# Kernel optimization log

Hardware: AMD Instinct MI355X
Metric: run time of the kernel (lower is better)

The kernel has to match this reference:

```python
import jax, jax.numpy as jnp
import numpy as np

HIDDEN = 512
VOCAB = 32000
BATCH = 64
SEQ = 256
N_LAYERS = 2
MAXLEN = 32


def setup_inputs() -> dict:
    key = jax.random.key(0)
    ks = jax.random.split(key, 8)
    s = 1.0 / np.sqrt(HIDDEN)
    return {
        "x": jax.random.randint(ks[0], (BATCH, SEQ), 0, VOCAB, dtype=jnp.int64),
        "emb": jax.random.normal(ks[1], (VOCAB, HIDDEN), jnp.float32),
        "W_ih": jax.random.uniform(ks[2], (N_LAYERS, HIDDEN, HIDDEN), jnp.float32, -s, s),
        "W_hh": jax.random.uniform(ks[3], (N_LAYERS, HIDDEN, HIDDEN), jnp.float32, -s, s),
        "b_ih": jax.random.uniform(ks[4], (N_LAYERS, HIDDEN), jnp.float32, -s, s),
        "b_hh": jax.random.uniform(ks[5], (N_LAYERS, HIDDEN), jnp.float32, -s, s),
        "W_fc": jax.random.uniform(ks[6], (VOCAB, HIDDEN), jnp.float32, -s, s),
        "b_fc": jax.random.uniform(ks[7], (VOCAB,), jnp.float32, -s, s),
    }


def _cell(h, x_t, W_ih, W_hh, b_ih, b_hh):
    # h: [L, B, H] stacked hidden; x_t: [B, H]. Multi-layer tanh Elman step.
    n_layers = W_ih.shape[0]
    inp = x_t
    new_h = []
    for l in range(n_layers):  # small fixed layer count
        hl = jnp.tanh(inp @ W_ih[l].T + b_ih[l] + h[l] @ W_hh[l].T + b_hh[l])
        new_h.append(hl)
        inp = hl
    return jnp.stack(new_h), inp


def reference(x, emb, W_ih, W_hh, b_ih, b_hh, W_fc, b_fc):
    B = x.shape[0]
    # ---- encoder: embed tokens, run stacked RNN over time ----
    xe = emb[x]  # [B, S, H]
    h0 = jnp.zeros((W_ih.shape[0], B, HIDDEN), emb.dtype)

    def enc_step(h, xt):
        h2, out = _cell(h, xt, W_ih, W_hh, b_ih, b_hh)
        return h2, out

    h_enc, _ = jax.lax.scan(enc_step, h0, jnp.swapaxes(xe, 0, 1))

    tok0 = jnp.zeros((B,), jnp.int32)

    def dec_step(carry, _):
        h, tok = carry
        e = emb[tok]  # [B, H]
        h2, out = _cell(h, e, W_ih, W_hh, b_ih, b_hh)
        logits = out @ W_fc.T + b_fc  # [B, V]
        nxt = jnp.argmax(logits, axis=-1).astype(jnp.int32)
        return (h2, nxt), logits

    (h_fin, _), logits = jax.lax.scan(dec_step, (h_enc, tok0), None, length=MAXLEN)
    vec_out = jnp.swapaxes(logits, 0, 1)  # [B, MAXLEN, V]
    return vec_out, h_fin
```

## Files before the change

### kernel.cpp

```cpp
#include <hip/hip_runtime.h>
#include <hip/hip_bf16.h>


typedef float v4f __attribute__((ext_vector_type(4)));
typedef short short8 __attribute__((ext_vector_type(8)));
typedef unsigned long long u64;

#define HID 512
#define NBAT 64
#define SEQL 256
#define NV 32000
#define TDEC 32
#define BH (64 * 512)
#define FPAD 32

__device__ __forceinline__ unsigned short f2bf(float f) {
  unsigned u = __float_as_uint(f);
  u = u + 0x7FFFu + ((u >> 16) & 1u);
  return (unsigned short)(u >> 16);
}
__device__ __forceinline__ unsigned fenc(float f) {
  unsigned u = __float_as_uint(f);
  return (u & 0x80000000u) ? ~u : (u | 0x80000000u);
}
__device__ __forceinline__ float ldf(const float* p) {
  return __hip_atomic_load(p, __ATOMIC_RELAXED, __HIP_MEMORY_SCOPE_AGENT);
}
__device__ __forceinline__ void stf(float* p, float v) {
  __hip_atomic_store(p, v, __ATOMIC_RELAXED, __HIP_MEMORY_SCOPE_AGENT);
}
__device__ __forceinline__ int ldflag(const int* p) {
  return __hip_atomic_load(p, __ATOMIC_RELAXED, __HIP_MEMORY_SCOPE_AGENT);
}
__device__ __forceinline__ void stflag(int* p, int v) {
  __hip_atomic_store(p, v, __ATOMIC_RELAXED, __HIP_MEMORY_SCOPE_AGENT);
}

__device__ __forceinline__ void wgbar(int* flags, int wg, int first, int count, unsigned ep) {
  __atomic_signal_fence(__ATOMIC_SEQ_CST);
  __builtin_amdgcn_s_waitcnt(0);
  __syncthreads();
  const int tid = threadIdx.x;
  if (tid == 0) stflag(&flags[wg * FPAD], (int)ep);
  int* rel = &flags[(256 + (first >> 5) + (count == 256 ? 8 : 0)) * FPAD];
  if (wg == first) {
    if (tid < 64) {
      for (int f = first + tid; f < first + count; f += 64) {
        while ((unsigned)ldflag(&flags[f * FPAD]) < ep) __builtin_amdgcn_s_sleep(1);
      }
    }
    __syncthreads();
    if (tid == 0) stflag(rel, (int)ep);
  } else if (tid == 0) {
    while ((unsigned)ldflag(rel) < ep) __builtin_amdgcn_s_sleep(4);
  }
  __atomic_signal_fence(__ATOMIC_SEQ_CST);
  __syncthreads();
}

__global__ void k_wfcb(const float* __restrict__ W, unsigned short* __restrict__ Wb) {
  const int n = NV * HID;
  for (int i = ((int)blockIdx.x * 256 + (int)threadIdx.x) * 8; i < n; i += 2048 * 256 * 8) {
    v4f a = *(const v4f*)(W + i);
    v4f b = *(const v4f*)(W + i + 4);
    short8 o;
    o[0] = (short)f2bf(a[0]); o[1] = (short)f2bf(a[1]);
    o[2] = (short)f2bf(a[2]); o[3] = (short)f2bf(a[3]);
    o[4] = (short)f2bf(b[0]); o[5] = (short)f2bf(b[1]);
    o[6] = (short)f2bf(b[2]); o[7] = (short)f2bf(b[3]);
    *(short8*)(Wb + i) = o;
  }
}

template <int GATHER>
__global__ __launch_bounds__(256, 2) void k_gemm(const float* __restrict__ A,
                                                 const int* __restrict__ xtok,
                                                 const float* __restrict__ emb,
                                                 const float* __restrict__ W,
                                                 const float* __restrict__ bias,
                                                 float* __restrict__ P) {
  __shared__ __align__(16) float As[32 * 132];
  __shared__ __align__(16) float Bs[32 * 132];
  const int tid = threadIdx.x;
  const int i0 = ((int)blockIdx.x >> 2) * 128, j0 = ((int)blockIdx.x & 3) * 128;
  const int tx = tid & 15, ty = tid >> 4;
  float acc[8][8] = {};
  const int sa = 4 * ((tx >> 2) & 1);
  const int sb = 4 * ((ty >> 2) & 1);
  const int pa0 = (tx * 8) ^ sa, pa1 = (tx * 8 + 4) ^ sa;
  const int pb0 = (ty * 8) ^ sb, pb1 = (ty * 8 + 4) ^ sb;
  for (int kc = 0; kc < HID; kc += 32) {
#pragma unroll
    for (int u = 0; u < 4; u++) {
      int lin = tid + u * 256;
      int il = lin >> 3, kq = (lin & 7) * 4;
      int pi = il ^ (4 * ((il >> 5) & 1));
      const float* asrc;
      if (GATHER) {
        int row = i0 + il;
        int tok = xtok[(row & 63) * SEQL + (row >> 6)];
        asrc = emb + (size_t)tok * HID + kc + kq;
      } else {
        asrc = A + (size_t)(i0 + il) * HID + kc + kq;
      }
      v4f av = *(const v4f*)asrc;
      v4f bv = *(const v4f*)(W + (size_t)(j0 + il) * HID + kc + kq);
      As[(kq + 0) * 132 + pi] = av[0]; As[(kq + 1) * 132 + pi] = av[1];
      As[(kq + 2) * 132 + pi] = av[2]; As[(kq + 3) * 132 + pi] = av[3];
      Bs[(kq + 0) * 132 + pi] = bv[0]; Bs[(kq + 1) * 132 + pi] = bv[1];
      Bs[(kq + 2) * 132 + pi] = bv[2]; Bs[(kq + 3) * 132 + pi] = bv[3];
    }
    __syncthreads();
#pragma unroll 8
    for (int k = 0; k < 32; k++) {
      v4f a0 = *(const v4f*)&As[k * 132 + pa0];
      v4f a1 = *(const v4f*)&As[k * 132 + pa1];
      v4f b0 = *(const v4f*)&Bs[k * 132 + pb0];
      v4f b1 = *(const v4f*)&Bs[k * 132 + pb1];
      float ar[8] = {a0[0], a0[1], a0[2], a0[3], a1[0], a1[1], a1[2], a1[3]};
      float br[8] = {b0[0], b0[1], b0[2], b0[3], b1[0], b1[1], b1[2], b1[3]};
#pragma unroll
      for (int r = 0; r < 8; r++)
#pragma unroll
        for (int c = 0; c < 8; c++) acc[r][c] = fmaf(ar[r], br[c], acc[r][c]);
    }
    __syncthreads();
  }
  v4f bl0 = *(const v4f*)(bias + j0 + ty * 8);
  v4f bl1 = *(const v4f*)(bias + j0 + ty * 8 + 4);
#pragma unroll
  for (int r = 0; r < 8; r++) {
    float* dst = P + (size_t)(i0 + tx * 8 + r) * HID + j0 + ty * 8;
    v4f o0 = {acc[r][0] + bl0[0], acc[r][1] + bl0[1], acc[r][2] + bl0[2], acc[r][3] + bl0[3]};
    v4f o1 = {acc[r][4] + bl1[0], acc[r][5] + bl1[1], acc[r][6] + bl1[2], acc[r][7] + bl1[3]};
    *(v4f*)dst = o0;
    *(v4f*)(dst + 4) = o1;
  }
}

__global__ __launch_bounds__(256, 2) void k_scan(float* __restrict__ P,
                                                 const float* __restrict__ Whh,
                                                 const float* __restrict__ bhh,
                                                 float* __restrict__ hbuf,
                                                 int* __restrict__ flags, int store_h,
                                                 unsigned ep) {
  __shared__ __align__(16) float hs[32 * 132];
  const int wg = blockIdx.x, tid = threadIdx.x;
  const int bg = wg >> 5, jg = wg & 31;
  const int b0 = bg * 8, j0 = jg * 16;
  const int bh = tid & 1, jg2 = (tid >> 1) & 3, ks = tid >> 3;
  v4f wv[4][4];
#pragma unroll
  for (int jj = 0; jj < 4; jj++)
#pragma unroll
    for (int i4 = 0; i4 < 4; i4++)
      wv[jj][i4] = *(const v4f*)(Whh + (size_t)(j0 + jg2 * 4 + jj) * HID + ks * 16 + i4 * 4);
  for (int t = 0; t < SEQL; t++) {
    const int p = t & 1;
    float* Pt = P + (size_t)t * BH;
    const float* hsrc = hbuf + p * BH + b0 * HID;
#pragma unroll
    for (int u = 0; u < 16; u++) {
      int lin = tid + u * 256;
      int b = lin >> 9, k = lin & 511;
      hs[(k >> 4) * 132 + b * 16 + (k & 15)] = ldf(hsrc + b * HID + k);
    }
    __syncthreads();
    float acc[4][4] = {};
#pragma unroll
    for (int i4 = 0; i4 < 4; i4++) {
#pragma unroll
      for (int bb = 0; bb < 4; bb++) {
        int b = bh * 4 + bb;
        v4f hv = *(const v4f*)&hs[ks * 132 + b * 16 + i4 * 4];
#pragma unroll
        for (int jj = 0; jj < 4; jj++) {
          float a = acc[bb][jj];
          a = fmaf(hv[0], wv[jj][i4][0], a);
          a = fmaf(hv[1], wv[jj][i4][1], a);
          a = fmaf(hv[2], wv[jj][i4][2], a);
          a = fmaf(hv[3], wv[jj][i4][3], a);
          acc[bb][jj] = a;
        }
      }
    }
    __syncthreads();
#pragma unroll
    for (int bb = 0; bb < 4; bb++) {
      v4f pv = {acc[bb][0], acc[bb][1], acc[bb][2], acc[bb][3]};
      *(v4f*)&hs[ks * 132 + (bh * 4 + bb) * 16 + jg2 * 4] = pv;
    }
    __syncthreads();
    if (tid < 128) {
      int bb = tid >> 4, jj = tid & 15;
      float sum = 0.f;
#pragma unroll
      for (int k2 = 0; k2 < 32; k2++) sum += hs[k2 * 132 + bb * 16 + jj];
      int jglob = j0 + jj, bglob = b0 + bb;
      float z = Pt[bglob * HID + jglob] + bhh[jglob] + sum;
      float h = tanhf(z);
      stf(&hbuf[(p ^ 1) * BH + bglob * HID + jglob], h);
      if (store_h) Pt[bglob * HID + jglob] = h;
    }
    wgbar(flags, wg, bg * 32, 32, ++ep);
  }
}

__device__ __forceinline__ void issue_tile(const unsigned short* __restrict__ Wfcb,
                                           float* buf, int wg, int tid, int T) {
  const int wv = tid >> 6, ln = tid & 63;
  const unsigned short* sb =
      Wfcb + (size_t)(wg * 128 + wv * 32 + (ln & 15)) * HID + T * 128 + (ln >> 4) * 8;
#pragma unroll
  for (int kc = 0; kc < 4; kc++)
#pragma unroll
    for (int fq = 0; fq < 2; fq++)
      __builtin_amdgcn_global_load_lds(
          (const unsigned int*)(sb + (size_t)fq * 16 * HID + kc * 32),
          (unsigned int*)(buf + wv * 2048 + kc * 512 + fq * 256), 16, 0, 0);
}

template <int PH>
__global__ __launch_bounds__(256, 1) void k_cell(
    const float* __restrict__ emb, const float* __restrict__ Wih,
    const float* __restrict__ Whh, const float* __restrict__ bih,
    const float* __restrict__ bhh, const u64* __restrict__ best,
    float* __restrict__ h0buf, float* __restrict__ h1buf,
    unsigned short* __restrict__ h1bf, int st) {
  __shared__ __align__(16) float Wl[2 * 4224];
  __shared__ __align__(16) float es[32 * 268];
  __shared__ __align__(16) float hss[32 * 268];
  const int wg = blockIdx.x, tid = threadIdx.x;
  const int bg = wg >> 6, jgD = wg & 63;
  const int bh = tid & 3, jg2 = (tid >> 2) & 1, ks = tid >> 3;
  const int p = st & 1;
#pragma unroll
  for (int m = 0; m < 2; m++) {
    const float* src = (m ? Whh : Wih) + (size_t)PH * HID * HID;
#pragma unroll
    for (int u = 0; u < 4; u++) {
      int lin = tid + u * 256;
      int j = lin >> 7, k4 = (lin & 127) * 4;
      v4f v = *(const v4f*)(src + (size_t)(jgD * 8 + j) * HID + k4);
      *(v4f*)&Wl[m * 4224 + (k4 >> 4) * 132 + j * 16 + (k4 & 15)] = v;
    }
  }
  if (PH == 0) {
#pragma unroll
    for (int u = 0; u < 8; u++) {
      int lin = tid + u * 256;
      int b = lin >> 7, k4 = (lin & 127) * 4;
      unsigned vtok = 0u;
      if (st > 0) {
        u64 kk = best[bg * 16 + b];
        vtok = 0xFFFFFFFFu - (unsigned)(kk & 0xFFFFFFFFull);
        if (vtok >= (unsigned)NV) vtok = 0u;
      }
      v4f av = *(const v4f*)(emb + (size_t)vtok * HID + k4);
      *(v4f*)&es[(k4 >> 4) * 268 + b * 16 + (k4 & 15)] = av;
    }
#pragma unroll
    for (int u = 0; u < 32; u++) {
      int lin = tid + u * 256;
      int b = lin >> 9, k = lin & 511;
      hss[(k >> 4) * 268 + b * 16 + (k & 15)] = h0buf[p * BH + (bg * 16 + b) * HID + k];
    }
  } else {
#pragma unroll
    for (int u = 0; u < 32; u++) {
      int lin = tid + u * 256;
      int b = lin >> 9, k = lin & 511;
      int off = (k >> 4) * 268 + b * 16 + (k & 15);
      int row = (bg * 16 + b) * HID + k;
      es[off] = h0buf[(p ^ 1) * BH + row];
      hss[off] = h1buf[p * BH + row];
    }
  }
  __syncthreads();
  float acc[4][4] = {};
  const float* Wi = &Wl[0];
  const float* Wh = &Wl[4224];
#pragma unroll
  for (int i4 = 0; i4 < 4; i4++) {
    v4f wi[4], wh[4];
#pragma unroll
    for (int jj = 0; jj < 4; jj++) {
      wi[jj] = *(const v4f*)&Wi[ks * 132 + (jg2 * 4 + jj) * 16 + i4 * 4];
      wh[jj] = *(const v4f*)&Wh[ks * 132 + (jg2 * 4 + jj) * 16 + i4 * 4];
    }
#pragma unroll
    for (int bb = 0; bb < 4; bb++) {
      int b = bh * 4 + bb;
      v4f evv = *(const v4f*)&es[ks * 268 + b * 16 + i4 * 4];
      v4f hvv = *(const v4f*)&hss[ks * 268 + b * 16 + i4 * 4];
#pragma unroll
      for (int jj = 0; jj < 4; jj++) {
        float a = acc[bb][jj];
        a = fmaf(evv[0], wi[jj][0], a); a = fmaf(evv[1], wi[jj][1], a);
        a = fmaf(evv[2], wi[jj][2], a); a = fmaf(evv[3], wi[jj][3], a);
        a = fmaf(hvv[0], wh[jj][0], a); a = fmaf(hvv[1], wh[jj][1], a);
        a = fmaf(hvv[2], wh[jj][2], a); a = fmaf(hvv[3], wh[jj][3], a);
        acc[bb][jj] = a;
      }
    }
  }
  __syncthreads();
#pragma unroll
  for (int bb = 0; bb < 4; bb++) {
    v4f pv = {acc[bb][0], acc[bb][1], acc[bb][2], acc[bb][3]};
    *(v4f*)&es[ks * 132 + (bh * 4 + bb) * 8 + jg2 * 4] = pv;
  }
  __syncthreads();
  if (tid < 128) {
    int b = tid >> 3, j = tid & 7;
    float sum = 0.f;
#pragma unroll
    for (int k2 = 0; k2 < 32; k2++) sum += es[k2 * 132 + b * 8 + j];
    int jglob = jgD * 8 + j, bglob = bg * 16 + b;
    float z = bih[PH * HID + jglob] + bhh[PH * HID + jglob] + sum;
    float h = tanhf(z);
    float* hb = (PH ? h1buf : h0buf);
    hb[(p ^ 1) * BH + bglob * HID + jglob] = h;
    if (PH) {
      unsigned hbv = f2bf(h);
      unsigned nb = (unsigned)__shfl_down((int)hbv, 1);
      if ((j & 1) == 0)
        *(unsigned*)(h1bf + (size_t)bglob * HID + jglob) = hbv | (nb << 16);
    }
  }
}

__global__ __launch_bounds__(256, 1) void k_logits(
    const unsigned short* __restrict__ Wfcb, const unsigned short* __restrict__ h1bf,
    const float* __restrict__ bfc, float* __restrict__ out, float* __restrict__ pmaxp,
    u64* __restrict__ best, int st) {
  __shared__ __align__(16) float tb0[8192];
  __shared__ __align__(16) float tb1[8192];
  __shared__ float pmr[256];
  const int wg = blockIdx.x, tid = threadIdx.x;
  if (wg == 250) {
    if (tid < 64) best[tid] = 0ull;
    return;
  }
  const int w = tid >> 6, lane = tid & 63;
  const int l16 = lane & 15, quad = lane >> 4;
  const int n0 = wg * 128 + w * 32;
  const int nc0 = n0 + l16, nc1 = n0 + 16 + l16;
  const float bf0 = bfc[nc0], bf1 = bfc[nc1];
  issue_tile(Wfcb, tb0, wg, tid, 0);
  v4f acc[4][2] = {};
#pragma unroll
  for (int t = 0; t < 4; t++) {
    __builtin_amdgcn_sched_barrier(0);
    const float* buf = (t & 1) ? tb1 : tb0;
    union { u64 q[2]; short8 s; } au[4][4];
#pragma unroll
    for (int mb = 0; mb < 4; mb++) {
      const unsigned short* hr = h1bf + (size_t)(mb * 16 + l16) * HID + t * 128 + quad * 8;
#pragma unroll
      for (int kc = 0; kc < 4; kc++) {
        au[mb][kc].q[0] = *(const u64*)(hr + kc * 32);
        au[mb][kc].q[1] = *(const u64*)(hr + kc * 32 + 4);
      }
    }
    __builtin_amdgcn_sched_barrier(0);
    if (t < 3) issue_tile(Wfcb, (t & 1) ? tb0 : tb1, wg, tid, t + 1);
    __builtin_amdgcn_sched_barrier(0);
    if (t < 3) asm volatile("s_waitcnt vmcnt(8)" ::: "memory");
    else       asm volatile("s_waitcnt vmcnt(0)" ::: "memory");
    __builtin_amdgcn_sched_barrier(0);
#pragma unroll
    for (int kc = 0; kc < 4; kc++) {
      short8 b0 = *(const short8*)(buf + w * 2048 + kc * 512 + lane * 4);
      short8 b1 = *(const short8*)(buf + w * 2048 + kc * 512 + 256 + lane * 4);
#pragma unroll
      for (int mb = 0; mb < 4; mb++) {
        acc[mb][0] =
            __builtin_amdgcn_mfma_f32_16x16x32_bf16(au[mb][kc].s, b0, acc[mb][0], 0, 0, 0);
        acc[mb][1] =
            __builtin_amdgcn_mfma_f32_16x16x32_bf16(au[mb][kc].s, b1, acc[mb][1], 0, 0, 0);
      }
    }
  }
#pragma unroll
  for (int mb = 0; mb < 4; mb++) {
#pragma unroll
    for (int r = 0; r < 4; r++) {
      float v0 = acc[mb][0][r] + bf0;
      float v1 = acc[mb][1][r] + bf1;
      int m = mb * 16 + quad * 4 + r;
      out[(size_t)(m * TDEC + st) * NV + nc0] = v0;
      out[(size_t)(m * TDEC + st) * NV + nc1] = v1;
      float mx = fmaxf(v0, v1);
      mx = fmaxf(mx, __shfl_xor(mx, 1));
      mx = fmaxf(mx, __shfl_xor(mx, 2));
      mx = fmaxf(mx, __shfl_xor(mx, 4));
      mx = fmaxf(mx, __shfl_xor(mx, 8));
      if (l16 == 0) pmr[w * 64 + m] = mx;
    }
  }
  __syncthreads();
  if (tid < 64) {
    float m4 = fmaxf(fmaxf(pmr[tid], pmr[64 + tid]), fmaxf(pmr[128 + tid], pmr[192 + tid]));
    pmaxp[tid * 256 + wg] = m4;
  }
}

__global__ __launch_bounds__(256, 1) void k_argmax(
    const float* __restrict__ Wfc, const float* __restrict__ bfc,
    const float* __restrict__ h1buf, const float* __restrict__ pmaxp,
    const float* __restrict__ out, u64* __restrict__ best, int st) {
  __shared__ __align__(16) float hcache[512];
  __shared__ float red[256];
  const int wg = blockIdx.x, tid = threadIdx.x;
  const int b = wg >> 2, q = wg & 3;
  const int p = st & 1;
  const float* hrow = h1buf + (p ^ 1) * BH + b * HID;
  hcache[tid] = hrow[tid];
  hcache[tid + 256] = hrow[tid + 256];
  red[tid] = (tid < 250) ? pmaxp[b * 256 + tid] : -3.0e38f;
  __syncthreads();
  for (int o = 128; o > 0; o >>= 1) {
    if (tid < o) red[tid] = fmaxf(red[tid], red[tid + o]);
    __syncthreads();
  }
  const float thr = red[0] - 0.05f;
  const size_t ob = (size_t)(b * TDEC + st) * NV + q * 8000;
  for (int i = tid * 2; i < 8000; i += 512) {
    u64 qq = *(const u64*)(out + ob + i);
    float lv[2] = {__uint_as_float((unsigned)qq), __uint_as_float((unsigned)(qq >> 32))};
#pragma unroll
    for (int c = 0; c < 2; c++) {
      if (lv[c] >= thr) {
        int vidx = q * 8000 + i + c;
        const v4f* h4 = (const v4f*)hcache;
        const v4f* w4 = (const v4f*)(Wfc + (size_t)vidx * HID);
        v4f s0 = 0, s1 = 0;
        for (int k = 0; k < 128; k += 2) {
          s0 += h4[k] * w4[k];
          s1 += h4[k + 1] * w4[k + 1];
        }
        v4f sv = s0 + s1;
        float d = bfc[vidx] + sv[0] + sv[1] + sv[2] + sv[3];
        u64 key = ((u64)fenc(d) << 32) | (u64)(0xFFFFFFFFu - (unsigned)vidx);
        atomicMax(&best[b], key);
      }
    }
  }
}

__global__ void k_hfin(const float* __restrict__ h0buf, const float* __restrict__ h1buf,
                       float* __restrict__ out) {
  int lin = (int)blockIdx.x * 256 + (int)threadIdx.x;
  int l = lin >> 15, r2 = lin & 32767;
  out[65536000 + lin] = (l ? h1buf : h0buf)[r2];
}

extern "C" void kernel_launch(void* const* d_in, const int* in_sizes, int n_in, void* d_out,
                              int out_size, void* d_ws, size_t ws_size, hipStream_t stream) {
  const int* x = (const int*)d_in[0];
  const float* emb = (const float*)d_in[1];
  const float* Wih = (const float*)d_in[2];
  const float* Whh = (const float*)d_in[3];
  const float* bih = (const float*)d_in[4];
  const float* bhh = (const float*)d_in[5];
  const float* Wfc = (const float*)d_in[6];
  const float* bfc = (const float*)d_in[7];
  float* out = (float*)d_out;
  char* ws = (char*)d_ws;

  float* P0 = (float*)ws;
  float* P1 = P0 + (size_t)SEQL * BH;
  unsigned short* Wfcb = (unsigned short*)(P1 + (size_t)SEQL * BH);
  char* small = (char*)(Wfcb + (size_t)NV * HID);
  float* h0buf = (float*)small;
  float* h1buf = h0buf + 2 * BH;
  unsigned short* h1bf = (unsigned short*)(h1buf + 2 * BH);
  float* pmaxp = (float*)(h1bf + BH);
  u64* best = (u64*)(pmaxp + 256 * 64);
  int* flags = (int*)(best + 64);
  size_t small_bytes = (size_t)2 * BH * 4 + (size_t)2 * BH * 4 + BH * 2 + 256 * 64 * 4 +
                       64 * 8 + (256 + 16) * FPAD * 4;

  hipMemsetAsync(small, 0, small_bytes, stream);
  k_wfcb<<<2048, 256, 0, stream>>>(Wfc, Wfcb);
  k_gemm<1><<<512, 256, 0, stream>>>(nullptr, x, emb, Wih, bih, P0);
  k_scan<<<256, 256, 0, stream>>>(P0, Whh, bhh, h0buf, flags, 1, 0u);
  k_gemm<0><<<512, 256, 0, stream>>>(P0, nullptr, nullptr, Wih + 262144, bih + 512, P1);
  k_scan<<<256, 256, 0, stream>>>(P1, Whh + 262144, bhh + 512, h1buf, flags, 0, 256u);
  for (int st = 0; st < TDEC; st++) {
    k_cell<0><<<256, 256, 0, stream>>>(emb, Wih, Whh, bih, bhh, best, h0buf, h1buf, h1bf, st);
    k_cell<1><<<256, 256, 0, stream>>>(emb, Wih, Whh, bih, bhh, best, h0buf, h1buf, h1bf, st);
    k_logits<<<251, 256, 0, stream>>>(Wfcb, h1bf, bfc, out, pmaxp, best, st);
    k_argmax<<<256, 256, 0, stream>>>(Wfc, bfc, h1buf, pmaxp, out, best, st);
  }
  k_hfin<<<256, 256, 0, stream>>>(h0buf, h1buf, out);
}
```

Before: 6.529 ms.

## Fuse both encoder RNN layers into one wavefront-pipelined persistent scan kernel

Replaces the two sequential layer scans and the intermediate layer-1 input GEMM with a single 512-workgroup persistent kernel. Layer 0 workgroups write hidden states into a 4-slot ring, and layer 1 workgroups consume them one step behind, computing the W_ih projection inline. Cross-layer flags give backpressure so the ring is not overwritten. This overlaps the two serial recurrences and removes a GEMM launch plus the P1 traffic. In exchange, layer 1 does extra per-step work, and the kernel relies on all 512 workgroups being co-resident for the spin barriers.

```diff
diff --git a/kernel.cpp b/kernel.cpp
--- a/kernel.cpp
+++ b/kernel.cpp
@@ -34,28 +34,6 @@
 }
 __device__ __forceinline__ void stflag(int* p, int v) {
   __hip_atomic_store(p, v, __ATOMIC_RELAXED, __HIP_MEMORY_SCOPE_AGENT);
-}
-
-__device__ __forceinline__ void wgbar(int* flags, int wg, int first, int count, unsigned ep) {
-  __atomic_signal_fence(__ATOMIC_SEQ_CST);
-  __builtin_amdgcn_s_waitcnt(0);
-  __syncthreads();
-  const int tid = threadIdx.x;
-  if (tid == 0) stflag(&flags[wg * FPAD], (int)ep);
-  int* rel = &flags[(256 + (first >> 5) + (count == 256 ? 8 : 0)) * FPAD];
-  if (wg == first) {
-    if (tid < 64) {
-      for (int f = first + tid; f < first + count; f += 64) {
-        while ((unsigned)ldflag(&flags[f * FPAD]) < ep) __builtin_amdgcn_s_sleep(1);
-      }
-    }
-    __syncthreads();
-    if (tid == 0) stflag(rel, (int)ep);
-  } else if (tid == 0) {
-    while ((unsigned)ldflag(rel) < ep) __builtin_amdgcn_s_sleep(4);
-  }
-  __atomic_signal_fence(__ATOMIC_SEQ_CST);
-  __syncthreads();
 }
 
 __global__ void k_wfcb(const float* __restrict__ W, unsigned short* __restrict__ Wb) {
@@ -138,71 +116,198 @@
   }
 }
 
-__global__ __launch_bounds__(256, 2) void k_scan(float* __restrict__ P,
-                                                 const float* __restrict__ Whh,
-                                                 const float* __restrict__ bhh,
-                                                 float* __restrict__ hbuf,
-                                                 int* __restrict__ flags, int store_h,
-                                                 unsigned ep) {
-  __shared__ __align__(16) float hs[32 * 132];
-  const int wg = blockIdx.x, tid = threadIdx.x;
+__global__ __launch_bounds__(256, 2) void k_scan2(
+    const float* __restrict__ P0, const float* __restrict__ Wih,
+    const float* __restrict__ Whh, const float* __restrict__ bih,
+    const float* __restrict__ bhh, float* __restrict__ h0ring,
+    float* __restrict__ h0buf, float* __restrict__ h1buf, int* __restrict__ flags) {
+  __shared__ __align__(16) float hs0[32 * 132];
+  __shared__ __align__(16) float hs1[32 * 132];
+  const int wgid = blockIdx.x, tid = threadIdx.x;
+  const int layer = wgid >> 8;
+  const int wg = wgid & 255;
   const int bg = wg >> 5, jg = wg & 31;
   const int b0 = bg * 8, j0 = jg * 16;
   const int bh = tid & 1, jg2 = (tid >> 1) & 3, ks = tid >> 3;
-  v4f wv[4][4];
-#pragma unroll
-  for (int jj = 0; jj < 4; jj++)
-#pragma unroll
-    for (int i4 = 0; i4 < 4; i4++)
-      wv[jj][i4] = *(const v4f*)(Whh + (size_t)(j0 + jg2 * 4 + jj) * HID + ks * 16 + i4 * 4);
-  for (int t = 0; t < SEQL; t++) {
-    const int p = t & 1;
-    float* Pt = P + (size_t)t * BH;
-    const float* hsrc = hbuf + p * BH + b0 * HID;
-#pragma unroll
-    for (int u = 0; u < 16; u++) {
-      int lin = tid + u * 256;
-      int b = lin >> 9, k = lin & 511;
-      hs[(k >> 4) * 132 + b * 16 + (k & 15)] = ldf(hsrc + b * HID + k);
-    }
-    __syncthreads();
-    float acc[4][4] = {};
-#pragma unroll
-    for (int i4 = 0; i4 < 4; i4++) {
+  int* arr = &flags[wgid * FPAD];
+  int* relA = &flags[(512 + bg) * FPAD];
+  int* relB = &flags[(520 + bg) * FPAD];
+
+  if (layer == 0) {
+    v4f wv[4][4];
+#pragma unroll
+    for (int jj = 0; jj < 4; jj++)
+#pragma unroll
+      for (int i4 = 0; i4 < 4; i4++)
+        wv[jj][i4] = *(const v4f*)(Whh + (size_t)(j0 + jg2 * 4 + jj) * HID + ks * 16 + i4 * 4);
+    for (int t = 0; t < SEQL; t++) {
+      const float* hsrc = h0ring + ((t + 3) & 3) * BH + b0 * HID;
+#pragma unroll
+      for (int u = 0; u < 16; u++) {
+        int lin = tid + u * 256;
+        int b = lin >> 9, k = lin & 511;
+        hs0[(k >> 4) * 132 + b * 16 + (k & 15)] = ldf(hsrc + b * HID + k);
+      }
+      __syncthreads();
+      float acc[4][4] = {};
+#pragma unroll
+      for (int i4 = 0; i4 < 4; i4++) {
+#pragma unroll
+        for (int bb = 0; bb < 4; bb++) {
+          int b = bh * 4 + bb;
+          v4f hv = *(const v4f*)&hs0[ks * 132 + b * 16 + i4 * 4];
+#pragma unroll
+          for (int jj = 0; jj < 4; jj++) {
+            float a = acc[bb][jj];
+            a = fmaf(hv[0], wv[jj][i4][0], a);
+            a = fmaf(hv[1], wv[jj][i4][1], a);
+            a = fmaf(hv[2], wv[jj][i4][2], a);
+            a = fmaf(hv[3], wv[jj][i4][3], a);
+            acc[bb][jj] = a;
+          }
+        }
+      }
+      __syncthreads();
 #pragma unroll
       for (int bb = 0; bb < 4; bb++) {
-        int b = bh * 4 + bb;
-        v4f hv = *(const v4f*)&hs[ks * 132 + b * 16 + i4 * 4];
-#pragma unroll
-        for (int jj = 0; jj < 4; jj++) {
-          float a = acc[bb][jj];
-          a = fmaf(hv[0], wv[jj][i4][0], a);
-          a = fmaf(hv[1], wv[jj][i4][1], a);
-          a = fmaf(hv[2], wv[jj][i4][2], a);
-          a = fmaf(hv[3], wv[jj][i4][3], a);
-          acc[bb][jj] = a;
+        v4f pv = {acc[bb][0], acc[bb][1], acc[bb][2], acc[bb][3]};
+        *(v4f*)&hs0[ks * 132 + (bh * 4 + bb) * 16 + jg2 * 4] = pv;
+      }
+      __syncthreads();
+      if (tid < 128) {
+        int bb = tid >> 4, jj = tid & 15;
+        float sum = 0.f;
+#pragma unroll
+        for (int k2 = 0; k2 < 32; k2++) sum += hs0[k2 * 132 + bb * 16 + jj];
+        int jglob = j0 + jj, bglob = b0 + bb;
+        float z = P0[(size_t)t * BH + bglob * HID + jglob] + bhh[jglob] + sum;
+        float h = tanhf(z);
+        stf(&h0ring[(t & 3) * BH + bglob * HID + jglob], h);
+        if (t == SEQL - 1) stf(&h0buf[bglob * HID + jglob], h);
+      }
+      unsigned ep = (unsigned)(t + 1);
+      __atomic_signal_fence(__ATOMIC_SEQ_CST);
+      __builtin_amdgcn_s_waitcnt(0);
+      __syncthreads();
+      if (tid == 0) stflag(arr, (int)ep);
+      if (jg == 0) {
+        if (tid < 32) {
+          while ((unsigned)ldflag(&flags[(bg * 32 + tid) * FPAD]) < ep)
+            __builtin_amdgcn_s_sleep(1);
+        } else if (tid == 32 && ep > 3) {
+          while ((unsigned)ldflag(relB) < ep - 3) __builtin_amdgcn_s_sleep(1);
         }
-      }
-    }
-    __syncthreads();
-#pragma unroll
-    for (int bb = 0; bb < 4; bb++) {
-      v4f pv = {acc[bb][0], acc[bb][1], acc[bb][2], acc[bb][3]};
-      *(v4f*)&hs[ks * 132 + (bh * 4 + bb) * 16 + jg2 * 4] = pv;
-    }
-    __syncthreads();
-    if (tid < 128) {
-      int bb = tid >> 4, jj = tid & 15;
-      float sum = 0.f;
-#pragma unroll
-      for (int k2 = 0; k2 < 32; k2++) sum += hs[k2 * 132 + bb * 16 + jj];
-      int jglob = j0 + jj, bglob = b0 + bb;
-      float z = Pt[bglob * HID + jglob] + bhh[jglob] + sum;
-      float h = tanhf(z);
-      stf(&hbuf[(p ^ 1) * BH + bglob * HID + jglob], h);
-      if (store_h) Pt[bglob * HID + jglob] = h;
-    }
-    wgbar(flags, wg, bg * 32, 32, ++ep);
+        __syncthreads();
+        if (tid == 0) stflag(relA, (int)ep);
+      } else if (tid == 0) {
+        while ((unsigned)ldflag(relA) < ep) __builtin_amdgcn_s_sleep(2);
+      }
+      __atomic_signal_fence(__ATOMIC_SEQ_CST);
+      __syncthreads();
+    }
+  } else {
+    v4f wvh[4][4], wvi[4][4];
+#pragma unroll
+    for (int jj = 0; jj < 4; jj++)
+#pragma unroll
+      for (int i4 = 0; i4 < 4; i4++) {
+        size_t off = (size_t)(j0 + jg2 * 4 + jj) * HID + ks * 16 + i4 * 4;
+        wvh[jj][i4] = *(const v4f*)(Whh + 262144 + off);
+        wvi[jj][i4] = *(const v4f*)(Wih + 262144 + off);
+      }
+    for (int t = 0; t < SEQL; t++) {
+      const int p1 = t & 1;
+      const float* h1src = h1buf + p1 * BH + b0 * HID;
+#pragma unroll
+      for (int u = 0; u < 16; u++) {
+        int lin = tid + u * 256;
+        int b = lin >> 9, k = lin & 511;
+        hs1[(k >> 4) * 132 + b * 16 + (k & 15)] = ldf(h1src + b * HID + k);
+      }
+      __syncthreads();
+      float acc[4][4] = {};
+#pragma unroll
+      for (int i4 = 0; i4 < 4; i4++) {
+#pragma unroll
+        for (int bb = 0; bb < 4; bb++) {
+          int b = bh * 4 + bb;
+          v4f hv = *(const v4f*)&hs1[ks * 132 + b * 16 + i4 * 4];
+#pragma unroll
+          for (int jj = 0; jj < 4; jj++) {
+            float a = acc[bb][jj];
+            a = fmaf(hv[0], wvh[jj][i4][0], a);
+            a = fmaf(hv[1], wvh[jj][i4][1], a);
+            a = fmaf(hv[2], wvh[jj][i4][2], a);
+            a = fmaf(hv[3], wvh[jj][i4][3], a);
+            acc[bb][jj] = a;
+          }
+        }
+      }
+      if (tid == 0) {
+        while ((unsigned)ldflag(relA) < (unsigned)(t + 1)) __builtin_amdgcn_s_sleep(2);
+      }
+      __atomic_signal_fence(__ATOMIC_SEQ_CST);
+      __syncthreads();
+      const float* h0src = h0ring + (t & 3) * BH + b0 * HID;
+#pragma unroll
+      for (int u = 0; u < 16; u++) {
+        int lin = tid + u * 256;
+        int b = lin >> 9, k = lin & 511;
+        hs0[(k >> 4) * 132 + b * 16 + (k & 15)] = ldf(h0src + b * HID + k);
+      }
+      __syncthreads();
+#pragma unroll
+      for (int i4 = 0; i4 < 4; i4++) {
+#pragma unroll
+        for (int bb = 0; bb < 4; bb++) {
+          int b = bh * 4 + bb;
+          v4f hv = *(const v4f*)&hs0[ks * 132 + b * 16 + i4 * 4];
+#pragma unroll
+          for (int jj = 0; jj < 4; jj++) {
+            float a = acc[bb][jj];
+            a = fmaf(hv[0], wvi[jj][i4][0], a);
+            a = fmaf(hv[1], wvi[jj][i4][1], a);
+            a = fmaf(hv[2], wvi[jj][i4][2], a);
+            a = fmaf(hv[3], wvi[jj][i4][3], a);
+            acc[bb][jj] = a;
+          }
+        }
+      }
+      __syncthreads();
+#pragma unroll
+      for (int bb = 0; bb < 4; bb++) {
+        v4f pv = {acc[bb][0], acc[bb][1], acc[bb][2], acc[bb][3]};
+        *(v4f*)&hs1[ks * 132 + (bh * 4 + bb) * 16 + jg2 * 4] = pv;
+      }
+      __syncthreads();
+      if (tid < 128) {
+        int bb = tid >> 4, jj = tid & 15;
+        float sum = 0.f;
+#pragma unroll
+        for (int k2 = 0; k2 < 32; k2++) sum += hs1[k2 * 132 + bb * 16 + jj];
+        int jglob = j0 + jj, bglob = b0 + bb;
+        float z = bih[HID + jglob] + bhh[HID + jglob] + sum;
+        float h = tanhf(z);
+        stf(&h1buf[(p1 ^ 1) * BH + bglob * HID + jglob], h);
+      }
+      unsigned ep = (unsigned)(t + 1);
+      __atomic_signal_fence(__ATOMIC_SEQ_CST);
+      __builtin_amdgcn_s_waitcnt(0);
+      __syncthreads();
+      if (tid == 0) stflag(arr, (int)ep);
+      if (jg == 0) {
+        if (tid < 32) {
+          while ((unsigned)ldflag(&flags[(256 + bg * 32 + tid) * FPAD]) < ep)
+            __builtin_amdgcn_s_sleep(1);
+        }
+        __syncthreads();
+        if (tid == 0) stflag(relB, (int)ep);
+      } else if (tid == 0) {
+        while ((unsigned)ldflag(relB) < ep) __builtin_amdgcn_s_sleep(2);
+      }
+      __atomic_signal_fence(__ATOMIC_SEQ_CST);
+      __syncthreads();
+    }
   }
 }
 
@@ -470,8 +575,9 @@
   char* ws = (char*)d_ws;
 
   float* P0 = (float*)ws;
-  float* P1 = P0 + (size_t)SEQL * BH;
-  unsigned short* Wfcb = (unsigned short*)(P1 + (size_t)SEQL * BH);
+  float* P1space = P0 + (size_t)SEQL * BH;
+  float* h0ring = P1space;
+  unsigned short* Wfcb = (unsigned short*)(P1space + (size_t)SEQL * BH);
   char* small = (char*)(Wfcb + (size_t)NV * HID);
   float* h0buf = (float*)small;
   float* h1buf = h0buf + 2 * BH;
@@ -480,14 +586,13 @@
   u64* best = (u64*)(pmaxp + 256 * 64);
   int* flags = (int*)(best + 64);
   size_t small_bytes = (size_t)2 * BH * 4 + (size_t)2 * BH * 4 + BH * 2 + 256 * 64 * 4 +
-                       64 * 8 + (256 + 16) * FPAD * 4;
+                       64 * 8 + (512 + 16) * FPAD * 4;
 
   hipMemsetAsync(small, 0, small_bytes, stream);
+  hipMemsetAsync(h0ring, 0, (size_t)4 * BH * 4, stream);
   k_wfcb<<<2048, 256, 0, stream>>>(Wfc, Wfcb);
   k_gemm<1><<<512, 256, 0, stream>>>(nullptr, x, emb, Wih, bih, P0);
-  k_scan<<<256, 256, 0, stream>>>(P0, Whh, bhh, h0buf, flags, 1, 0u);
-  k_gemm<0><<<512, 256, 0, stream>>>(P0, nullptr, nullptr, Wih + 262144, bih + 512, P1);
-  k_scan<<<256, 256, 0, stream>>>(P1, Whh + 262144, bhh + 512, h1buf, flags, 0, 256u);
+  k_scan2<<<512, 256, 0, stream>>>(P0, Wih, Whh, bih, bhh, h0ring, h0buf, h1buf, flags);
   for (int st = 0; st < TDEC; st++) {
     k_cell<0><<<256, 256, 0, stream>>>(emb, Wih, Whh, bih, bhh, best, h0buf, h1buf, h1bf, st);
     k_cell<1><<<256, 256, 0, stream>>>(emb, Wih, Whh, bih, bhh, best, h0buf, h1buf, h1bf, st);
```

New measurement: 5.635 ms. -13.7%, faster.
